# Kernel tuning notes

Measured on AMD Instinct MI355X. Metric: run time of the kernel, lower is better.

Reference implementation:

```python
import jax, jax.numpy as jnp
import numpy as np
from jax import lax

B, S, DM = 4, 4096, 1024
H, P, R = 16, 32, 8
D = DM // H  # head_dim = 64
K_SEL = 4


def setup_inputs() -> dict:
    key = jax.random.key(0)
    ks = jax.random.split(key, 6)
    x = jax.random.normal(ks[0], (B, S, DM), dtype=jnp.float32)
    K_state = jax.random.normal(ks[1], (H, P, R, D), dtype=jnp.float32) / np.sqrt(D)
    V_state = jax.random.normal(ks[2], (H, P, R, D), dtype=jnp.float32) / np.sqrt(D)
    W_router = jax.random.normal(ks[3], (H, D, P), dtype=jnp.float32) / np.sqrt(D)
    W_out = jax.random.normal(ks[4], (DM, DM), dtype=jnp.float32) / np.sqrt(DM)
    b_out = jnp.zeros((DM,), dtype=jnp.float32)
    return {"x": x, "K_state": K_state, "V_state": V_state,
            "W_router": W_router, "W_out": W_out, "b_out": b_out, "k": K_SEL}


def reference(x, K_state, V_state, W_router, W_out, b_out, k):
    b, s, dm = x.shape
    h, p, r, d = K_state.shape
    xh = x.reshape(b, s, h, d)  # per-head token features

    # Router: top-k partition selection per token per head.
    logits = jnp.einsum('bshd,hdp->bshp', xh, W_router)
    topv = lax.top_k(logits, k)[0]            # [b,s,h,k]
    thresh = topv[..., -1:]                   # k-th largest logit
    neg_inf = jnp.array(-jnp.inf, dtype=logits.dtype)
    gates = jax.nn.softmax(jnp.where(logits >= thresh, logits, neg_inf), axis=-1)  # [b,s,h,p], zero off top-k

    # Attention over state rows within each partition (masked-dense == sparse gather math).
    scale = jnp.asarray(1.0 / np.sqrt(d), dtype=x.dtype)
    scores = jnp.einsum('bshd,hprd->bshpr', xh, K_state) * scale
    attn = jax.nn.softmax(scores, axis=-1)    # softmax over rows r within a partition

    # Gate-weighted combine of per-partition attention outputs, fused to avoid [b,s,h,p,d].
    w = attn * gates[..., None]               # [b,s,h,p,r]
    heads = jnp.einsum('bshpr,hprd->bshd', w, V_state)

    out = heads.reshape(b, s, dm) @ W_out + b_out
    return out
```

## Files before the change

### kernel.cpp

```cpp
#include <hip/hip_runtime.h>
#include <hip/hip_bf16.h>

#define BB 4
#define SS 4096
#define DM 1024
#define HH 16
#define PP 32
#define RR 8
#define DD 64
#define NTOK (BB*SS)
#define MM NTOK
#define NN DM
#define KK DM

typedef __attribute__((ext_vector_type(8))) short short8;
typedef __attribute__((ext_vector_type(4))) float floatx4;

static __device__ inline short f2bf(float f) {
    union { __hip_bfloat16 b; short s; } u; u.b = __float2bfloat16(f); return u.s;
}
static __device__ inline short8 pack8(float4 lo, float4 hi) {
    short8 r;
    r[0] = f2bf(lo.x); r[1] = f2bf(lo.y); r[2] = f2bf(lo.z); r[3] = f2bf(lo.w);
    r[4] = f2bf(hi.x); r[5] = f2bf(hi.y); r[6] = f2bf(hi.z); r[7] = f2bf(hi.w);
    return r;
}

static __device__ inline unsigned bfr(float f) {
    unsigned u = __float_as_uint(f);
    return u + 0x7fffu + ((u >> 16) & 1u);
}
static __device__ inline int pk2(float a, float b) {
    return __builtin_amdgcn_perm(bfr(b), bfr(a), 0x07060302);
}
static __device__ inline short8 pk8(float4 lo, float4 hi) {
    union { short8 s; int i[4]; } r;
    r.i[0] = pk2(lo.x, lo.y); r.i[1] = pk2(lo.z, lo.w);
    r.i[2] = pk2(hi.x, hi.y); r.i[3] = pk2(hi.z, hi.w);
    return r.s;
}

__global__ __launch_bounds__(256) void convert_w(const float* __restrict__ Wo,
                                                 __hip_bfloat16* __restrict__ wsw) {
    int tid = blockIdx.x * 256 + threadIdx.x;
    int l = tid & 63;
    int kblk = (tid >> 6) & 31;
    int ntile = tid >> 11;
    int col = ntile * 16 + (l & 15);
    int krow = kblk * 32 + (l >> 4) * 8;
#pragma unroll
    for (int j = 0; j < 8; ++j) {
        wsw[(size_t)tid * 8 + j] = __float2bfloat16(Wo[(size_t)(krow + j) * NN + col]);
    }
}

__global__ __launch_bounds__(256) void convert_kv(const float* __restrict__ Kst,
                                                  const float* __restrict__ Vst,
                                                  __hip_bfloat16* __restrict__ kfrag,
                                                  __hip_bfloat16* __restrict__ vfrag) {
    int tid = blockIdx.x * 256 + threadIdx.x;
    int arr = tid >> 15;
    int idx = tid & 32767;
    int h = idx >> 11, blk = (idx >> 6) & 31, fl = idx & 63;
    int fm = fl & 15, fk = fl >> 4;
    short8 val;
    short* dst;
    if (arr == 0) {
        int mt = blk >> 1, kb = blk & 1;
        int pr = mt * 16 + fm, d0 = kb * 32 + fk * 8;
        const float* src = Kst + ((size_t)h * 256 + pr) * 64 + d0;
        float4 lo = *(const float4*)src, hi = *(const float4*)(src + 4);
        val = pack8(lo, hi);
        dst = (short*)kfrag + (size_t)idx * 8;
    } else {
        int mt = blk >> 3, kb = blk & 7;
        int d = mt * 16 + fm, pr0 = kb * 32 + fk * 8;
        const float* src = Vst + ((size_t)h * 256 + pr0) * 64 + d;
#pragma unroll
        for (int j = 0; j < 8; ++j) val[j] = f2bf(src[j * 64]);
        dst = (short*)vfrag + (size_t)idx * 8;
    }
    *(short8*)dst = val;
}

__global__ __launch_bounds__(256, 3) void attn_v7(const float* __restrict__ x,
                                                  const float* __restrict__ Wr,
                                                  const __hip_bfloat16* __restrict__ kfrag,
                                                  const __hip_bfloat16* __restrict__ vfrag,
                                                  const int* __restrict__ kp,
                                                  __hip_bfloat16* __restrict__ hb) {
    __shared__ __align__(16) char smem[40960];
    float (*xs)[68]     = (float (*)[68])smem;
    float (*Lg)[36]     = (float (*)[36])(smem + 17408);
    short* wf           = (short*)smem;
    float (*gatesT)[64] = (float (*)[64])(smem + 32768);

    const int lane = threadIdx.x & 63;
    const int w = threadIdx.x >> 6;
    const int l15 = lane & 15, l4 = lane >> 4;
    const int t0 = blockIdx.x * 64;
    const int h = blockIdx.y;

    {
        int row = threadIdx.x >> 2, q = threadIdx.x & 3;
        const float4* src = (const float4*)(x + (size_t)(t0 + row) * DM + h * 64 + q * 16);
        float4 v0 = src[0], v1 = src[1], v2 = src[2], v3 = src[3];
        float4* dst = (float4*)&xs[row][q * 16];
        dst[0] = v0; dst[1] = v1; dst[2] = v2; dst[3] = v3;
    }

    const int p = lane & 31, dh = lane >> 5;
    float wreg[32];
    {
        const float* wrp = Wr + (size_t)h * (DD * PP) + dh * 32 * PP + p;
#pragma unroll
        for (int dd = 0; dd < 32; ++dd) wreg[dd] = wrp[dd * PP];
    }
    const int kkv = kp[0];

    short8 xb[4][2];
#pragma unroll
    for (int nt = 0; nt < 4; ++nt)
#pragma unroll
        for (int kb = 0; kb < 2; ++kb) {
            const float* bp = x + (size_t)(t0 + nt * 16 + l15) * DM + h * 64 + kb * 32 + l4 * 8;
            float4 lo = *(const float4*)bp;
            float4 hi = *(const float4*)(bp + 4);
            xb[nt][kb] = pk8(lo, hi);
        }
    short8 ka[4][2];
#pragma unroll
    for (int mi = 0; mi < 4; ++mi)
#pragma unroll
        for (int kb = 0; kb < 2; ++kb)
            ka[mi][kb] = *(const short8*)((const short*)kfrag +
                          ((size_t)(h * 32 + (w * 4 + mi) * 2 + kb) * 512 + lane * 8));

    __syncthreads();

    floatx4 acc[4][4] = {};
#pragma unroll
    for (int kb = 0; kb < 2; ++kb)
#pragma unroll
        for (int mi = 0; mi < 4; ++mi)
#pragma unroll
            for (int nt = 0; nt < 4; ++nt)
                acc[mi][nt] = __builtin_amdgcn_mfma_f32_16x16x32_bf16(ka[mi][kb], xb[nt][kb], acc[mi][nt], 0, 0, 0);

    for (int it = 0; it < 16; it += 2) {
        const int ta = w * 16 + it;
        const int tb = ta + 1;
        float la = 0.f, lb = 0.f;
#pragma unroll
        for (int j = 0; j < 8; ++j) {
            float4 qa = *(const float4*)&xs[ta][dh * 32 + 4 * j];
            float4 qb = *(const float4*)&xs[tb][dh * 32 + 4 * j];
            la += qa.x * wreg[4 * j];     lb += qb.x * wreg[4 * j];
            la += qa.y * wreg[4 * j + 1]; lb += qb.y * wreg[4 * j + 1];
            la += qa.z * wreg[4 * j + 2]; lb += qb.z * wreg[4 * j + 2];
            la += qa.w * wreg[4 * j + 3]; lb += qb.w * wreg[4 * j + 3];
        }
        la += __shfl_xor(la, 32);
        lb += __shfl_xor(lb, 32);
        if (lane < 32) {
            Lg[ta][lane] = la;
            Lg[tb][lane] = lb;
        }
    }
    __syncthreads();

    float thresh = 0.f, a1 = 0.f;
    if (lane < 16) {
        int t = w * 16 + lane;
        float lgr[32];
        const float4* lrow = (const float4*)&Lg[t][0];
#pragma unroll
        for (int c = 0; c < 8; ++c) {
            float4 q4 = lrow[c];
            lgr[4 * c] = q4.x; lgr[4 * c + 1] = q4.y; lgr[4 * c + 2] = q4.z; lgr[4 * c + 3] = q4.w;
        }
        float aa = -INFINITY, b2 = -INFINITY, c3 = -INFINITY, d4 = -INFINITY;
#pragma unroll
        for (int pp = 0; pp < 32; ++pp) {
            float v = lgr[pp];
            float na = fmaxf(aa, v); v = fminf(aa, v); aa = na;
            float nb = fmaxf(b2, v); v = fminf(b2, v); b2 = nb;
            float nc = fmaxf(c3, v); v = fminf(c3, v); c3 = nc;
            d4 = fmaxf(d4, v);
        }
        thresh = (kkv >= 4) ? d4 : (kkv == 3 ? c3 : (kkv == 2 ? b2 : aa));
        a1 = aa;
    }
    thresh = __shfl(thresh, l15);
    a1     = __shfl(a1, l15);

    {
        const int t = w * 16 + l15;
        const int p8 = l4 * 8;
        const float4* lrow = (const float4*)&Lg[t][p8];
        float4 qa = lrow[0], qb = lrow[1];
        float e0 = (qa.x >= thresh) ? __expf(qa.x - a1) : 0.f;
        float e1 = (qa.y >= thresh) ? __expf(qa.y - a1) : 0.f;
        float e2 = (qa.z >= thresh) ? __expf(qa.z - a1) : 0.f;
        float e3 = (qa.w >= thresh) ? __expf(qa.w - a1) : 0.f;
        float e4 = (qb.x >= thresh) ? __expf(qb.x - a1) : 0.f;
        float e5 = (qb.y >= thresh) ? __expf(qb.y - a1) : 0.f;
        float e6 = (qb.z >= thresh) ? __expf(qb.z - a1) : 0.f;
        float e7 = (qb.w >= thresh) ? __expf(qb.w - a1) : 0.f;
        float part = ((e0 + e1) + (e2 + e3)) + ((e4 + e5) + (e6 + e7));
        part += __shfl_xor(part, 16);
        part += __shfl_xor(part, 32);
        float inv = 1.f / part;
        gatesT[p8 + 0][t] = e0 * inv;
        gatesT[p8 + 1][t] = e1 * inv;
        gatesT[p8 + 2][t] = e2 * inv;
        gatesT[p8 + 3][t] = e3 * inv;
        gatesT[p8 + 4][t] = e4 * inv;
        gatesT[p8 + 5][t] = e5 * inv;
        gatesT[p8 + 6][t] = e6 * inv;
        gatesT[p8 + 7][t] = e7 * inv;
    }
    __syncthreads();

#pragma unroll
    for (int mi = 0; mi < 4; ++mi) {
        const int mt = w * 4 + mi;
        const int pidx = mt * 2 + (l4 >> 1);
#pragma unroll
        for (int nt = 0; nt < 4; ++nt) {
            float g = gatesT[pidx][nt * 16 + l15];
            float s0 = acc[mi][nt][0] * 0.125f;
            float s1 = acc[mi][nt][1] * 0.125f;
            float s2 = acc[mi][nt][2] * 0.125f;
            float s3 = acc[mi][nt][3] * 0.125f;
            float mx = fmaxf(fmaxf(s0, s1), fmaxf(s2, s3));
            mx = fmaxf(mx, __shfl_xor(mx, 16));
            float e0 = __expf(s0 - mx), e1 = __expf(s1 - mx);
            float e2 = __expf(s2 - mx), e3 = __expf(s3 - mx);
            float loc = (e0 + e1) + (e2 + e3);
            float se = loc + __shfl_xor(loc, 16);
            float ws = g / se;
            int2 pk;
            pk.x = pk2(e0 * ws, e1 * ws);
            pk.y = pk2(e2 * ws, e3 * ws);
            int off = (((mt & 1) * 2 + (l4 >> 1)) * 16 + l15) * 8 + (l4 & 1) * 4;
            *(int2*)&wf[(nt * 8 + (mt >> 1)) * 512 + off] = pk;
        }
    }
    __syncthreads();

    floatx4 h4[4] = {};
#pragma unroll
    for (int kb = 0; kb < 8; ++kb) {
        short8 va = *(const short8*)((const short*)vfrag +
                      ((size_t)(h * 32 + w * 8 + kb) * 512 + lane * 8));
#pragma unroll
        for (int nt = 0; nt < 4; ++nt) {
            short8 wb = *(const short8*)&wf[(nt * 8 + kb) * 512 + lane * 8];
            h4[nt] = __builtin_amdgcn_mfma_f32_16x16x32_bf16(va, wb, h4[nt], 0, 0, 0);
        }
    }
#pragma unroll
    for (int nt = 0; nt < 4; ++nt) {
        int t = t0 + nt * 16 + l15;
        int2 pk;
        pk.x = pk2(h4[nt][0], h4[nt][1]);
        pk.y = pk2(h4[nt][2], h4[nt][3]);
        *(int2*)((short*)hb + (size_t)t * DM + h * 64 + w * 16 + l4 * 4) = pk;
    }
}

__global__ __launch_bounds__(256) void gemm_v3(const __hip_bfloat16* __restrict__ Abf,
                                               const __hip_bfloat16* __restrict__ Bsw,
                                               const float* __restrict__ bias,
                                               float* __restrict__ C) {
    __shared__ __align__(16) short As[2][4096];
    const int lane = threadIdx.x & 63;
    const int wave = threadIdx.x >> 6;
    const int wm = wave >> 1, wn = wave & 1;

    const int wg  = blockIdx.y * 8 + blockIdx.x;
    const int xcd = wg & 7;
    const int loc = wg >> 3;
    const int bm0 = (xcd * 16 + (loc >> 3)) * 128;
    const int bn0 = (loc & 7) * 128;

    const int l15 = lane & 15, l4 = lane >> 4;

    const short* Ap = (const short*)Abf;
    const short* Bp = (const short*)Bsw;

    const int c0 = (wave * 2 + 0) * 64 + lane;
    const int c1 = (wave * 2 + 1) * 64 + lane;
    const short* g0 = Ap + (size_t)(bm0 + (c0 >> 2)) * KK + (c0 & 3) * 8;
    const short* g1 = Ap + (size_t)(bm0 + (c1 >> 2)) * KK + (c1 & 3) * 8;

    int boff[4];
#pragma unroll
    for (int nt = 0; nt < 4; ++nt)
        boff[nt] = (((bn0 >> 4) + wn * 4 + nt) * 32) * 512 + lane * 8;

    int aoff[4];
#pragma unroll
    for (int mt = 0; mt < 4; ++mt)
        aoff[mt] = ((wm * 64 + mt * 16 + l15) * 4 + l4) * 8;

    floatx4 acc[4][4] = {};

    __builtin_amdgcn_global_load_lds(
        (const __attribute__((address_space(1))) unsigned int*)(g0),
        (__attribute__((address_space(3))) unsigned int*)&As[0][(wave * 2 + 0) * 512], 16, 0, 0);
    __builtin_amdgcn_global_load_lds(
        (const __attribute__((address_space(1))) unsigned int*)(g1),
        (__attribute__((address_space(3))) unsigned int*)&As[0][(wave * 2 + 1) * 512], 16, 0, 0);
    short8 bcur[4], bnxt[4];
#pragma unroll
    for (int nt = 0; nt < 4; ++nt)
        bcur[nt] = *(const short8*)(Bp + boff[nt]);
    __syncthreads();

    for (int kb = 0; kb < 32; ++kb) {
        const int cur = kb & 1;
        const int nxt = cur ^ 1;
        if (kb < 31) {
            __builtin_amdgcn_global_load_lds(
                (const __attribute__((address_space(1))) unsigned int*)(g0 + (kb + 1) * 32),
                (__attribute__((address_space(3))) unsigned int*)&As[nxt][(wave * 2 + 0) * 512], 16, 0, 0);
            __builtin_amdgcn_global_load_lds(
                (const __attribute__((address_space(1))) unsigned int*)(g1 + (kb + 1) * 32),
                (__attribute__((address_space(3))) unsigned int*)&As[nxt][(wave * 2 + 1) * 512], 16, 0, 0);
#pragma unroll
            for (int nt = 0; nt < 4; ++nt)
                bnxt[nt] = *(const short8*)(Bp + boff[nt] + (kb + 1) * 512);
        }
        short8 a[4];
#pragma unroll
        for (int mt = 0; mt < 4; ++mt)
            a[mt] = *(const short8*)&As[cur][aoff[mt]];
#pragma unroll
        for (int mt = 0; mt < 4; ++mt)
#pragma unroll
            for (int nt = 0; nt < 4; ++nt)
                acc[mt][nt] = __builtin_amdgcn_mfma_f32_16x16x32_bf16(a[mt], bcur[nt], acc[mt][nt], 0, 0, 0);
        __syncthreads();
#pragma unroll
        for (int nt = 0; nt < 4; ++nt)
            bcur[nt] = bnxt[nt];
    }

#pragma unroll
    for (int nt = 0; nt < 4; ++nt) {
        const int col = bn0 + wn * 64 + nt * 16 + l15;
        const float bv = bias[col];
#pragma unroll
        for (int mt = 0; mt < 4; ++mt) {
            const int row0 = bm0 + wm * 64 + mt * 16 + l4 * 4;
#pragma unroll
            for (int i = 0; i < 4; ++i)
                C[(size_t)(row0 + i) * NN + col] = acc[mt][nt][i] + bv;
        }
    }
}

extern "C" void kernel_launch(void* const* d_in, const int* in_sizes, int n_in,
                              void* d_out, int out_size, void* d_ws, size_t ws_size,
                              hipStream_t stream) {
    const float* x   = (const float*)d_in[0];
    const float* Kst = (const float*)d_in[1];
    const float* Vst = (const float*)d_in[2];
    const float* Wr  = (const float*)d_in[3];
    const float* Wo  = (const float*)d_in[4];
    const float* bo  = (const float*)d_in[5];
    const int*   kp  = (const int*)d_in[6];
    float* out = (float*)d_out;

    __hip_bfloat16* hb    = (__hip_bfloat16*)d_ws;
    __hip_bfloat16* wsw   = hb + (size_t)MM * KK;
    __hip_bfloat16* kfrag = wsw + (size_t)KK * NN;
    __hip_bfloat16* vfrag = kfrag + 16 * 32 * 512;

    convert_w<<<dim3(512), 256, 0, stream>>>(Wo, wsw);
    convert_kv<<<dim3(256), 256, 0, stream>>>(Kst, Vst, kfrag, vfrag);
    attn_v7<<<dim3(NTOK / 64, HH), 256, 0, stream>>>(x, Wr, kfrag, vfrag, kp, hb);
    gemm_v3<<<dim3(NN / 128, MM / 128), 256, 0, stream>>>(hb, wsw, bo, out);
}
```

Before: 249.5 us.

## Split attention block work across 8 waves instead of 4

The attention kernel now runs with 512 threads (8 waves) per block instead of 256. Every phase is re-partitioned across the extra waves: the scores MFMA covers 2 m-tiles per wave, router logits and gates use 8 tokens per wave, and the V combine is split by head-dim tile and token pair. The aim is lower register pressure per wave and more waves in flight to hide memory latency. In exchange each block carries more redundant per-wave work (each wave loads the router weights and x fragments) and more threads take part in the barriers.

```diff
diff --git a/kernel.cpp b/kernel.cpp
--- a/kernel.cpp
+++ b/kernel.cpp
@@ -83,30 +83,31 @@
     *(short8*)dst = val;
 }
 
-__global__ __launch_bounds__(256, 3) void attn_v7(const float* __restrict__ x,
-                                                  const float* __restrict__ Wr,
-                                                  const __hip_bfloat16* __restrict__ kfrag,
-                                                  const __hip_bfloat16* __restrict__ vfrag,
-                                                  const int* __restrict__ kp,
-                                                  __hip_bfloat16* __restrict__ hb) {
+__global__ __launch_bounds__(512, 4) void attn_v8b(const float* __restrict__ x,
+                                                   const float* __restrict__ Wr,
+                                                   const __hip_bfloat16* __restrict__ kfrag,
+                                                   const __hip_bfloat16* __restrict__ vfrag,
+                                                   const int* __restrict__ kp,
+                                                   __hip_bfloat16* __restrict__ hb) {
     __shared__ __align__(16) char smem[40960];
     float (*xs)[68]     = (float (*)[68])smem;
     float (*Lg)[36]     = (float (*)[36])(smem + 17408);
     short* wf           = (short*)smem;
     float (*gatesT)[64] = (float (*)[64])(smem + 32768);
 
-    const int lane = threadIdx.x & 63;
-    const int w = threadIdx.x >> 6;
+    const int tid = threadIdx.x;
+    const int lane = tid & 63;
+    const int w = tid >> 6;
     const int l15 = lane & 15, l4 = lane >> 4;
     const int t0 = blockIdx.x * 64;
     const int h = blockIdx.y;
 
     {
-        int row = threadIdx.x >> 2, q = threadIdx.x & 3;
-        const float4* src = (const float4*)(x + (size_t)(t0 + row) * DM + h * 64 + q * 16);
-        float4 v0 = src[0], v1 = src[1], v2 = src[2], v3 = src[3];
-        float4* dst = (float4*)&xs[row][q * 16];
-        dst[0] = v0; dst[1] = v1; dst[2] = v2; dst[3] = v3;
+        int row = tid >> 3, q = tid & 7;
+        const float4* src = (const float4*)(x + (size_t)(t0 + row) * DM + h * 64 + q * 8);
+        float4 v0 = src[0], v1 = src[1];
+        float4* dst = (float4*)&xs[row][q * 8];
+        dst[0] = v0; dst[1] = v1;
     }
 
     const int p = lane & 31, dh = lane >> 5;
@@ -118,37 +119,33 @@
     }
     const int kkv = kp[0];
 
-    short8 xb[4][2];
-#pragma unroll
-    for (int nt = 0; nt < 4; ++nt)
-#pragma unroll
-        for (int kb = 0; kb < 2; ++kb) {
+    floatx4 acc[2][4] = {};
+#pragma unroll
+    for (int kb = 0; kb < 2; ++kb) {
+        short8 xbk[4];
+#pragma unroll
+        for (int nt = 0; nt < 4; ++nt) {
             const float* bp = x + (size_t)(t0 + nt * 16 + l15) * DM + h * 64 + kb * 32 + l4 * 8;
             float4 lo = *(const float4*)bp;
             float4 hi = *(const float4*)(bp + 4);
-            xb[nt][kb] = pk8(lo, hi);
-        }
-    short8 ka[4][2];
-#pragma unroll
-    for (int mi = 0; mi < 4; ++mi)
-#pragma unroll
-        for (int kb = 0; kb < 2; ++kb)
-            ka[mi][kb] = *(const short8*)((const short*)kfrag +
-                          ((size_t)(h * 32 + (w * 4 + mi) * 2 + kb) * 512 + lane * 8));
-
-    __syncthreads();
-
-    floatx4 acc[4][4] = {};
-#pragma unroll
-    for (int kb = 0; kb < 2; ++kb)
-#pragma unroll
-        for (int mi = 0; mi < 4; ++mi)
+            xbk[nt] = pk8(lo, hi);
+        }
+        short8 kak[2];
+#pragma unroll
+        for (int mi = 0; mi < 2; ++mi)
+            kak[mi] = *(const short8*)((const short*)kfrag +
+                       ((size_t)(h * 32 + (w * 2 + mi) * 2 + kb) * 512 + lane * 8));
+#pragma unroll
+        for (int mi = 0; mi < 2; ++mi)
 #pragma unroll
             for (int nt = 0; nt < 4; ++nt)
-                acc[mi][nt] = __builtin_amdgcn_mfma_f32_16x16x32_bf16(ka[mi][kb], xb[nt][kb], acc[mi][nt], 0, 0, 0);
-
-    for (int it = 0; it < 16; it += 2) {
-        const int ta = w * 16 + it;
+                acc[mi][nt] = __builtin_amdgcn_mfma_f32_16x16x32_bf16(kak[mi], xbk[nt], acc[mi][nt], 0, 0, 0);
+    }
+
+    __syncthreads();
+
+    for (int it = 0; it < 8; it += 2) {
+        const int ta = w * 8 + it;
         const int tb = ta + 1;
         float la = 0.f, lb = 0.f;
 #pragma unroll
@@ -170,8 +167,8 @@
     __syncthreads();
 
     float thresh = 0.f, a1 = 0.f;
-    if (lane < 16) {
-        int t = w * 16 + lane;
+    if (lane < 8) {
+        int t = w * 8 + lane;
         float lgr[32];
         const float4* lrow = (const float4*)&Lg[t][0];
 #pragma unroll
@@ -191,40 +188,32 @@
         thresh = (kkv >= 4) ? d4 : (kkv == 3 ? c3 : (kkv == 2 ? b2 : aa));
         a1 = aa;
     }
-    thresh = __shfl(thresh, l15);
-    a1     = __shfl(a1, l15);
+    thresh = __shfl(thresh, lane & 7);
+    a1     = __shfl(a1, lane & 7);
 
     {
-        const int t = w * 16 + l15;
-        const int p8 = l4 * 8;
-        const float4* lrow = (const float4*)&Lg[t][p8];
-        float4 qa = lrow[0], qb = lrow[1];
+        const int t = w * 8 + (lane & 7);
+        const int p4 = (lane >> 3) * 4;
+        float4 qa = *(const float4*)&Lg[t][p4];
         float e0 = (qa.x >= thresh) ? __expf(qa.x - a1) : 0.f;
         float e1 = (qa.y >= thresh) ? __expf(qa.y - a1) : 0.f;
         float e2 = (qa.z >= thresh) ? __expf(qa.z - a1) : 0.f;
         float e3 = (qa.w >= thresh) ? __expf(qa.w - a1) : 0.f;
-        float e4 = (qb.x >= thresh) ? __expf(qb.x - a1) : 0.f;
-        float e5 = (qb.y >= thresh) ? __expf(qb.y - a1) : 0.f;
-        float e6 = (qb.z >= thresh) ? __expf(qb.z - a1) : 0.f;
-        float e7 = (qb.w >= thresh) ? __expf(qb.w - a1) : 0.f;
-        float part = ((e0 + e1) + (e2 + e3)) + ((e4 + e5) + (e6 + e7));
+        float part = (e0 + e1) + (e2 + e3);
+        part += __shfl_xor(part, 8);
         part += __shfl_xor(part, 16);
         part += __shfl_xor(part, 32);
         float inv = 1.f / part;
-        gatesT[p8 + 0][t] = e0 * inv;
-        gatesT[p8 + 1][t] = e1 * inv;
-        gatesT[p8 + 2][t] = e2 * inv;
-        gatesT[p8 + 3][t] = e3 * inv;
-        gatesT[p8 + 4][t] = e4 * inv;
-        gatesT[p8 + 5][t] = e5 * inv;
-        gatesT[p8 + 6][t] = e6 * inv;
-        gatesT[p8 + 7][t] = e7 * inv;
-    }
-    __syncthreads();
-
-#pragma unroll
-    for (int mi = 0; mi < 4; ++mi) {
-        const int mt = w * 4 + mi;
+        gatesT[p4 + 0][t] = e0 * inv;
+        gatesT[p4 + 1][t] = e1 * inv;
+        gatesT[p4 + 2][t] = e2 * inv;
+        gatesT[p4 + 3][t] = e3 * inv;
+    }
+    __syncthreads();
+
+#pragma unroll
+    for (int mi = 0; mi < 2; ++mi) {
+        const int mt = w * 2 + mi;
         const int pidx = mt * 2 + (l4 >> 1);
 #pragma unroll
         for (int nt = 0; nt < 4; ++nt) {
@@ -249,24 +238,26 @@
     }
     __syncthreads();
 
-    floatx4 h4[4] = {};
+    const int dt = w & 3;
+    const int nt0 = (w >> 2) * 2;
+    floatx4 h4[2] = {};
 #pragma unroll
     for (int kb = 0; kb < 8; ++kb) {
         short8 va = *(const short8*)((const short*)vfrag +
-                      ((size_t)(h * 32 + w * 8 + kb) * 512 + lane * 8));
-#pragma unroll
-        for (int nt = 0; nt < 4; ++nt) {
-            short8 wb = *(const short8*)&wf[(nt * 8 + kb) * 512 + lane * 8];
-            h4[nt] = __builtin_amdgcn_mfma_f32_16x16x32_bf16(va, wb, h4[nt], 0, 0, 0);
-        }
-    }
-#pragma unroll
-    for (int nt = 0; nt < 4; ++nt) {
-        int t = t0 + nt * 16 + l15;
+                      ((size_t)(h * 32 + dt * 8 + kb) * 512 + lane * 8));
+#pragma unroll
+        for (int j = 0; j < 2; ++j) {
+            short8 wb = *(const short8*)&wf[((nt0 + j) * 8 + kb) * 512 + lane * 8];
+            h4[j] = __builtin_amdgcn_mfma_f32_16x16x32_bf16(va, wb, h4[j], 0, 0, 0);
+        }
+    }
+#pragma unroll
+    for (int j = 0; j < 2; ++j) {
+        int t = t0 + (nt0 + j) * 16 + l15;
         int2 pk;
-        pk.x = pk2(h4[nt][0], h4[nt][1]);
-        pk.y = pk2(h4[nt][2], h4[nt][3]);
-        *(int2*)((short*)hb + (size_t)t * DM + h * 64 + w * 16 + l4 * 4) = pk;
+        pk.x = pk2(h4[j][0], h4[j][1]);
+        pk.y = pk2(h4[j][2], h4[j][3]);
+        *(int2*)((short*)hb + (size_t)t * DM + h * 64 + dt * 16 + l4 * 4) = pk;
     }
 }
 
@@ -381,6 +372,6 @@
 
     convert_w<<<dim3(512), 256, 0, stream>>>(Wo, wsw);
     convert_kv<<<dim3(256), 256, 0, stream>>>(Kst, Vst, kfrag, vfrag);
-    attn_v7<<<dim3(NTOK / 64, HH), 256, 0, stream>>>(x, Wr, kfrag, vfrag, kp, hb);
+    attn_v8b<<<dim3(NTOK / 64, HH), 512, 0, stream>>>(x, Wr, kfrag, vfrag, kp, hb);
     gemm_v3<<<dim3(NN / 128, MM / 128), 256, 0, stream>>>(hb, wsw, bo, out);
 }
```

After: 257.2 us. +3.1%, slower.
